# Kernel optimization log

Hardware: AMD Instinct MI355X
Metric: run time of the kernel (lower is better)

Reference implementation:

```python
import jax, jax.numpy as jnp
import numpy as np

B, Q, K, D, H, HD, OUT = 4, 1024, 1024, 256, 8, 32, 256


def setup_inputs() -> dict:
    key = jax.random.key(0)
    ks = jax.random.split(key, 11)
    s = 0.05  # small init scale for weights
    return {
        "q_data": jax.random.normal(ks[0], (B, Q, D), jnp.float32),
        "m_data": jax.random.normal(ks[1], (B, K, D), jnp.float32),
        "bias": jax.random.normal(ks[2], (B, 1, 1, K), jnp.float32),
        "nonbatched_bias": jax.random.normal(ks[3], (H, Q, K), jnp.float32),
        "query_w": jax.random.normal(ks[4], (D, H, HD), jnp.float32) * s,
        "key_w": jax.random.normal(ks[5], (D, H, HD), jnp.float32) * s,
        "value_w": jax.random.normal(ks[6], (D, H, HD), jnp.float32) * s,
        "gating_w": jax.random.normal(ks[7], (D, H, HD), jnp.float32) * s,
        "gating_b": jnp.ones((H, HD), jnp.float32),
        "output_w": jax.random.normal(ks[8], (H, HD, OUT), jnp.float32) * s,
        "output_b": jnp.zeros((OUT,), jnp.float32),
    }


def reference(q_data, m_data, bias, nonbatched_bias, query_w, key_w, value_w,
              gating_w, gating_b, output_w, output_b):
    key_dim = query_w.shape[-1]
    # QKV projections; queries pre-scaled by 1/sqrt(head_dim)
    q = jnp.einsum('bqa,ahc->bqhc', q_data, query_w) * key_dim ** (-0.5)
    k = jnp.einsum('bka,ahc->bkhc', m_data, key_w)
    v = jnp.einsum('bka,ahc->bkhc', m_data, value_w)
    # attention logits [b,h,q,k] plus batched and nonbatched additive biases
    logits_update = jnp.einsum('bqhc,bkhc->bhqk', q, k)
    logits = logits_update + bias + nonbatched_bias[None]
    weights = jax.nn.softmax(logits, axis=-1)
    weighted_avg = jnp.einsum('bhqk,bkhc->bqhc', weights, v)
    # sigmoid gating on the value-aggregated output
    gate = jax.nn.sigmoid(jnp.einsum('bqc,chv->bqhv', q_data, gating_w) + gating_b)
    weighted_avg = weighted_avg * gate
    output = jnp.einsum('bqhc,hco->bqo', weighted_avg, output_w) + output_b
    return (output, logits_update)
```

## Files before the change

kernel.cpp:

```cpp
#include <hip/hip_runtime.h>
#include <hip/hip_bf16.h>

#define NB 4
#define NQ 1024
#define NKS 1024
#define ND 256
#define NH 8
#define NHD 32
#define NOUT 256
#define SPLIT 4

typedef __attribute__((ext_vector_type(8))) short v8s;
typedef __attribute__((ext_vector_type(4))) short v4s;
typedef __attribute__((ext_vector_type(4))) float f32x4;

__global__ __launch_bounds__(256) void prep_all(
    const float* __restrict__ qd, const float* __restrict__ md,
    const float* __restrict__ qw, const float* __restrict__ kw,
    const float* __restrict__ vw, const float* __restrict__ gw,
    const float* __restrict__ ow,
    __hip_bfloat16* __restrict__ Abf, __hip_bfloat16* __restrict__ Wt)
{
  if (blockIdx.x < 1024) {
    const int gid = blockIdx.x * 256 + threadIdx.x;
    const float* src = (gid < 131072) ? qd : md;
    const size_t off = (size_t)(gid & 131071) * 8;
    const float4 a = ((const float4*)(src + off))[0];
    const float4 c = ((const float4*)(src + off))[1];
    __hip_bfloat16 t8[8];
    t8[0]=__float2bfloat16(a.x); t8[1]=__float2bfloat16(a.y);
    t8[2]=__float2bfloat16(a.z); t8[3]=__float2bfloat16(a.w);
    t8[4]=__float2bfloat16(c.x); t8[5]=__float2bfloat16(c.y);
    t8[6]=__float2bfloat16(c.z); t8[7]=__float2bfloat16(c.w);
    *(v8s*)(Abf + (size_t)gid * 8) = *(v8s*)t8;
    return;
  }
  __shared__ float tile[64][65];
  const int wb = blockIdx.x - 1024;
  const int m = wb >> 4, bx = wb & 15;
  const float* src = (m == 0) ? qw : (m == 1) ? kw : (m == 2) ? vw
                   : (m == 3) ? gw : ow;
  const float scale = (m == 0) ? 0.1767766952966369f : 1.0f;
  const int d0 = (bx >> 2) * 64, o0 = (bx & 3) * 64;
  #pragma unroll
  for (int i = 0; i < 16; ++i) {
    const int idx = threadIdx.x + i * 256;
    tile[idx >> 6][idx & 63] = src[(size_t)(d0 + (idx >> 6)) * 256 + o0 + (idx & 63)];
  }
  __syncthreads();
  __hip_bfloat16* dst = Wt + (size_t)m * 65536;
  #pragma unroll
  for (int i = 0; i < 16; ++i) {
    const int idx = threadIdx.x + i * 256;
    const int orow = idx >> 6, dc = idx & 63;
    dst[(size_t)(o0 + orow) * 256 + d0 + dc] = __float2bfloat16(tile[dc][orow] * scale);
  }
}

__global__ __launch_bounds__(256) void proj_kernel(
    const __hip_bfloat16* __restrict__ Abf, const __hip_bfloat16* __restrict__ Wt,
    const float* __restrict__ gating_b,
    __hip_bfloat16* __restrict__ Qw, __hip_bfloat16* __restrict__ Kw,
    __hip_bfloat16* __restrict__ Vt, float* __restrict__ G)
{
  const int wv = threadIdx.x >> 6, lane = threadIdx.x & 63;
  const int c = lane & 15, g = lane >> 4;
  const int task = blockIdx.x * 4 + wv;
  const int ctg = task & 3;
  const int mat = (task >> 2) & 1;
  const int r0g = (task >> 3) & 255;
  const int src = task >> 11;
  const int r0 = r0g * 16;
  const int b = r0 >> 10, pos0 = r0 & 1023;
  const f32x4 z = {0.f, 0.f, 0.f, 0.f};

  const __hip_bfloat16* A = Abf + ((size_t)src * 4096 + r0) * 256;
  v8s af[8];
  #pragma unroll
  for (int ks = 0; ks < 8; ++ks)
    af[ks] = *(const v8s*)(A + c * 256 + ks * 32 + g * 8);

  const int widx = (src == 0) ? (mat ? 3 : 0) : (mat ? 2 : 1);
  const __hip_bfloat16* W = Wt + (size_t)widx * 65536;
  const bool swapped = (src == 1) && (mat == 1);

  f32x4 ac[4] = {z, z, z, z};
  #pragma unroll
  for (int ks = 0; ks < 8; ++ks) {
    #pragma unroll
    for (int j = 0; j < 4; ++j) {
      v8s wf = *(const v8s*)(W + (size_t)((ctg * 4 + j) * 16 + c) * 256 + ks * 32 + g * 8);
      ac[j] = swapped
        ? __builtin_amdgcn_mfma_f32_16x16x32_bf16(wf, af[ks], ac[j], 0, 0, 0)
        : __builtin_amdgcn_mfma_f32_16x16x32_bf16(af[ks], wf, ac[j], 0, 0, 0);
    }
  }

  if (src == 0 && mat == 0) {
    #pragma unroll
    for (int j = 0; j < 4; ++j) {
      const int o = (ctg * 4 + j) * 16 + c, h = o >> 5, hd = o & 31;
      #pragma unroll
      for (int r = 0; r < 4; ++r)
        Qw[((size_t)(b * NH + h) * 1024 + pos0 + 4 * g + r) * 32 + hd] =
            __float2bfloat16(ac[j][r]);
    }
  } else if (src == 0) {
    #pragma unroll
    for (int j = 0; j < 4; ++j) {
      const int o = (ctg * 4 + j) * 16 + c;
      const float gb = gating_b[o];
      #pragma unroll
      for (int r = 0; r < 4; ++r)
        G[(size_t)(r0 + 4 * g + r) * 256 + o] = ac[j][r] + gb;
    }
  } else if (mat == 0) {
    #pragma unroll
    for (int j = 0; j < 4; ++j) {
      const int o = (ctg * 4 + j) * 16 + c, h = o >> 5, hd = o & 31;
      #pragma unroll
      for (int r = 0; r < 4; ++r)
        Kw[((size_t)(b * NH + h) * 1024 + pos0 + 4 * g + r) * 32 + hd] =
            __float2bfloat16(ac[j][r]);
    }
  } else {
    #pragma unroll
    for (int j = 0; j < 4; ++j) {
      #pragma unroll
      for (int r = 0; r < 4; ++r) {
        const int o2 = (ctg * 4 + j) * 16 + 4 * g + r;
        Vt[((size_t)(b * NH + (o2 >> 5)) * 32 + (o2 & 31)) * 1024 + pos0 + c] =
            __float2bfloat16(ac[j][r]);
      }
    }
  }
}

__global__ __launch_bounds__(256) void attn_kernel(
    const __hip_bfloat16* __restrict__ Qw, const __hip_bfloat16* __restrict__ Kw,
    const __hip_bfloat16* __restrict__ Vt,
    const float* __restrict__ bias, const float* __restrict__ nbb,
    float* __restrict__ out_logits,
    __hip_bfloat16* __restrict__ partO, float* __restrict__ partL)
{
  __shared__ __align__(16) __hip_bfloat16 sP[4][16][72];

  const int wv = threadIdx.x >> 6, lane = threadIdx.x & 63;
  const int c = lane & 15, g = lane >> 4;
  const int xcd   = blockIdx.x & 7;
  const int slot  = blockIdx.x >> 3;
  const int bh    = ((slot >> 6) << 3) | xcd;
  const int inner = slot & 63;
  const int sp    = inner >> 4;
  const int qtg   = inner & 15;
  const int qt  = qtg * 4 + wv;
  const int b = bh >> 3, h = bh & 7;
  const int rem = bh * 64 + qt;
  const int q0 = qt * 16;
  const int kbase = sp * (NKS / SPLIT);
  const size_t bhs = (size_t)bh;

  const __hip_bfloat16* Kbase = Kw + bhs * NKS * NHD;
  const __hip_bfloat16* Vbase = Vt + bhs * NHD * NKS;
  const float* biasb = bias + (size_t)b * NKS;
  const float* nbbb  = nbb + ((size_t)h * NQ + q0) * NKS;

  const v8s qfrag = *(const v8s*)(Qw + (bhs * NQ + q0 + c) * NHD + g * 8);

  const f32x4 zacc = {0.f, 0.f, 0.f, 0.f};
  f32x4 O0 = zacc, O1 = zacc;
  float lsumL[4] = {0.f, 0.f, 0.f, 0.f};

  auto loadKV = [&](int k0, v8s* kf, v8s* vf) {
    kf[0] = *(const v8s*)(Kbase + (k0 +      c) * NHD + g * 8);
    kf[1] = *(const v8s*)(Kbase + (k0 + 16 + c) * NHD + g * 8);
    kf[2] = *(const v8s*)(Kbase + (k0 + 32 + c) * NHD + g * 8);
    kf[3] = *(const v8s*)(Kbase + (k0 + 48 + c) * NHD + g * 8);
    vf[0] = *(const v8s*)(Vbase + (     c) * NKS + k0 +      g * 8);
    vf[1] = *(const v8s*)(Vbase + (16 + c) * NKS + k0 +      g * 8);
    vf[2] = *(const v8s*)(Vbase + (     c) * NKS + k0 + 32 + g * 8);
    vf[3] = *(const v8s*)(Vbase + (16 + c) * NKS + k0 + 32 + g * 8);
  };
  auto loadBias = [&](int k0, float* bn) {
    #pragma unroll
    for (int t = 0; t < 4; ++t) {
      const float bvt = biasb[k0 + t * 16 + c];
      #pragma unroll
      for (int r = 0; r < 4; ++r)
        bn[t * 4 + r] = bvt + nbbb[(g * 4 + r) * NKS + k0 + t * 16 + c];
    }
  };

  auto compute = [&](int k0, const v8s* kf, const v8s* vf, const float* bn) {
    f32x4 S[4];
    #pragma unroll
    for (int t = 0; t < 4; ++t)
      S[t] = __builtin_amdgcn_mfma_f32_16x16x32_bf16(qfrag, kf[t], zacc, 0, 0, 0);

    #pragma unroll
    for (int r = 0; r < 4; ++r) {
      const int qrow = q0 + g * 4 + r;
      float* lp = out_logits + (bhs * NQ + qrow) * (size_t)NKS + k0 + c;
      float psum = 0.f;
      #pragma unroll
      for (int t = 0; t < 4; ++t) {
        __builtin_nontemporal_store(S[t][r], lp + t * 16);
        const float p = __expf(S[t][r] + bn[t * 4 + r]);
        psum += p;
        sP[wv][g * 4 + r][t * 16 + c] = __float2bfloat16(p);
      }
      lsumL[r] += psum;
    }

    const v8s pa0 = *(const v8s*)&sP[wv][c][g * 8];
    const v8s pa1 = *(const v8s*)&sP[wv][c][32 + g * 8];
    O0 = __builtin_amdgcn_mfma_f32_16x16x32_bf16(pa0, vf[0], O0, 0, 0, 0);
    O0 = __builtin_amdgcn_mfma_f32_16x16x32_bf16(pa1, vf[2], O0, 0, 0, 0);
    O1 = __builtin_amdgcn_mfma_f32_16x16x32_bf16(pa0, vf[1], O1, 0, 0, 0);
    O1 = __builtin_amdgcn_mfma_f32_16x16x32_bf16(pa1, vf[3], O1, 0, 0, 0);
  };

  v8s kfA[4], vfA[4], kfB[4], vfB[4];
  float bnA[16], bnB[16];

  loadKV(kbase, kfA, vfA);
  loadBias(kbase, bnA);
  #pragma unroll 1
  for (int kt = 0; kt < NKS / SPLIT / 64; kt += 2) {
    loadKV(kbase + (kt + 1) * 64, kfB, vfB);
    loadBias(kbase + (kt + 1) * 64, bnB);
    compute(kbase + kt * 64, kfA, vfA, bnA);
    if (kt + 2 < NKS / SPLIT / 64) {
      loadKV(kbase + (kt + 2) * 64, kfA, vfA);
      loadBias(kbase + (kt + 2) * 64, bnA);
    }
    compute(kbase + (kt + 1) * 64, kfB, vfB, bnB);
  }

  #pragma unroll
  for (int r = 0; r < 4; ++r) {
    float rs = lsumL[r];
    rs += __shfl_xor(rs, 1);
    rs += __shfl_xor(rs, 2);
    rs += __shfl_xor(rs, 4);
    rs += __shfl_xor(rs, 8);
    const int row = 4 * g + r;
    const size_t pb = ((size_t)(rem * SPLIT + sp) * 16 + row) * 32;
    partO[pb + c]      = __float2bfloat16(O0[r]);
    partO[pb + 16 + c] = __float2bfloat16(O1[r]);
    if (c == 0) partL[(size_t)(rem * SPLIT + sp) * 16 + row] = rs;
  }
}

__global__ __launch_bounds__(256) void outproj_kernel(
    const __hip_bfloat16* __restrict__ partO, const float* __restrict__ partL,
    const float* __restrict__ G, const __hip_bfloat16* __restrict__ WtO,
    const float* __restrict__ output_b, float* __restrict__ out)
{
  __shared__ __align__(16) __hip_bfloat16 sRows[16][264];
  const int t = threadIdx.x;
  const int wv = t >> 6, lane = t & 63;
  const int c = lane & 15, g = lane >> 4;
  const int r0 = blockIdx.x * 16;
  const int b = r0 >> 10, qt = (r0 & 1023) >> 4;
  const int h = t >> 5, hd = t & 31;
  const int rem = (b * NH + h) * 64 + qt;

  #pragma unroll 4
  for (int row = 0; row < 16; ++row) {
    float o = 0.f, l = 0.f;
    #pragma unroll
    for (int sp = 0; sp < SPLIT; ++sp) {
      const size_t base = (size_t)(rem * SPLIT + sp) * 16 + row;
      o += __bfloat162float(partO[base * 32 + hd]);
      l += partL[base];
    }
    const float gl = G[(size_t)(r0 + row) * 256 + t];
    sRows[row][t] = __float2bfloat16((o / l) * (1.f / (1.f + __expf(-gl))));
  }
  __syncthreads();

  const f32x4 z = {0.f, 0.f, 0.f, 0.f};
  f32x4 ac[4] = {z, z, z, z};
  #pragma unroll
  for (int ks = 0; ks < 8; ++ks) {
    const v8s af = *(const v8s*)&sRows[c][ks * 32 + g * 8];
    #pragma unroll
    for (int j = 0; j < 4; ++j) {
      const v8s wf = *(const v8s*)(WtO + (size_t)((wv * 4 + j) * 16 + c) * 256 + ks * 32 + g * 8);
      ac[j] = __builtin_amdgcn_mfma_f32_16x16x32_bf16(af, wf, ac[j], 0, 0, 0);
    }
  }
  #pragma unroll
  for (int j = 0; j < 4; ++j) {
    const int o = (wv * 4 + j) * 16 + c;
    const float ob = output_b[o];
    #pragma unroll
    for (int r = 0; r < 4; ++r)
      out[(size_t)(r0 + 4 * g + r) * 256 + o] = ac[j][r] + ob;
  }
}

extern "C" void kernel_launch(void* const* d_in, const int* in_sizes, int n_in,
                              void* d_out, int out_size, void* d_ws, size_t ws_size,
                              hipStream_t stream) {
  const float* q_data   = (const float*)d_in[0];
  const float* m_data   = (const float*)d_in[1];
  const float* bias     = (const float*)d_in[2];
  const float* nbb      = (const float*)d_in[3];
  const float* query_w  = (const float*)d_in[4];
  const float* key_w    = (const float*)d_in[5];
  const float* value_w  = (const float*)d_in[6];
  const float* gating_w = (const float*)d_in[7];
  const float* gating_b = (const float*)d_in[8];
  const float* output_w = (const float*)d_in[9];
  const float* output_b = (const float*)d_in[10];

  float* out        = (float*)d_out;
  float* out_logits = out + (size_t)NB * NQ * NOUT;

  char* ws = (char*)d_ws;
  const size_t MB = 1u << 20;
  __hip_bfloat16* Qw  = (__hip_bfloat16*)(ws);
  __hip_bfloat16* Kw  = (__hip_bfloat16*)(ws + 2 * MB);
  __hip_bfloat16* Vt  = (__hip_bfloat16*)(ws + 4 * MB);
  float*          G   = (float*)(ws + 6 * MB);
  __hip_bfloat16* Abf = (__hip_bfloat16*)(ws + 10 * MB);
  __hip_bfloat16* partO = (__hip_bfloat16*)(ws + 10 * MB);
  float*          partL = (float*)(ws + 19 * MB);
  __hip_bfloat16* Wt  = (__hip_bfloat16*)(ws + 20 * MB);

  prep_all<<<1104, 256, 0, stream>>>(q_data, m_data, query_w, key_w, value_w,
                                     gating_w, output_w, Abf, Wt);
  proj_kernel<<<1024, 256, 0, stream>>>(Abf, Wt, gating_b, Qw, Kw, Vt, G);
  attn_kernel<<<2048, 256, 0, stream>>>(Qw, Kw, Vt, bias, nbb, out_logits, partO, partL);
  outproj_kernel<<<256, 256, 0, stream>>>(partO, partL, G, Wt + (size_t)4 * 65536,
                                          output_b, out);
}
```

Before: 85.33 us.

## Transpose QK^T MFMA so each lane owns one query row for vectorized I/O

The QK^T MFMA operands are swapped so the accumulator comes out transposed: each lane holds four consecutive keys for a single query row instead of four query rows for one key. This turns the logits stores, bias and nonbatched-bias loads, and the P writes to shared memory into 16-byte or 8-byte vector accesses rather than scalar strided ones. The row-sum reduction shrinks to two cross-lane shuffles. The trade-off is a different LDS write pattern for sP, which may cause bank conflicts, and per-lane row addressing that must still match the PV MFMA layout.

```diff
diff --git a/kernel.cpp b/kernel.cpp
--- a/kernel.cpp
+++ b/kernel.cpp
@@ -163,13 +163,14 @@
   const __hip_bfloat16* Kbase = Kw + bhs * NKS * NHD;
   const __hip_bfloat16* Vbase = Vt + bhs * NHD * NKS;
   const float* biasb = bias + (size_t)b * NKS;
-  const float* nbbb  = nbb + ((size_t)h * NQ + q0) * NKS;
+  const float* nbbq  = nbb + ((size_t)h * NQ + q0 + c) * NKS;
+  float*       logq  = out_logits + (bhs * NQ + q0 + c) * (size_t)NKS;
 
   const v8s qfrag = *(const v8s*)(Qw + (bhs * NQ + q0 + c) * NHD + g * 8);
 
   const f32x4 zacc = {0.f, 0.f, 0.f, 0.f};
   f32x4 O0 = zacc, O1 = zacc;
-  float lsumL[4] = {0.f, 0.f, 0.f, 0.f};
+  float lsum = 0.f;
 
   auto loadKV = [&](int k0, v8s* kf, v8s* vf) {
     kf[0] = *(const v8s*)(Kbase + (k0 +      c) * NHD + g * 8);
@@ -181,35 +182,37 @@
     vf[2] = *(const v8s*)(Vbase + (     c) * NKS + k0 + 32 + g * 8);
     vf[3] = *(const v8s*)(Vbase + (16 + c) * NKS + k0 + 32 + g * 8);
   };
-  auto loadBias = [&](int k0, float* bn) {
+  auto loadBias = [&](int k0, f32x4* bn) {
     #pragma unroll
     for (int t = 0; t < 4; ++t) {
-      const float bvt = biasb[k0 + t * 16 + c];
-      #pragma unroll
-      for (int r = 0; r < 4; ++r)
-        bn[t * 4 + r] = bvt + nbbb[(g * 4 + r) * NKS + k0 + t * 16 + c];
+      const f32x4 b4 = *(const f32x4*)(biasb + k0 + t * 16 + 4 * g);
+      const f32x4 n4 = *(const f32x4*)(nbbq  + k0 + t * 16 + 4 * g);
+      bn[t] = b4 + n4;
     }
   };
 
-  auto compute = [&](int k0, const v8s* kf, const v8s* vf, const float* bn) {
+  auto compute = [&](int k0, const v8s* kf, const v8s* vf, const f32x4* bn) {
     f32x4 S[4];
     #pragma unroll
     for (int t = 0; t < 4; ++t)
-      S[t] = __builtin_amdgcn_mfma_f32_16x16x32_bf16(qfrag, kf[t], zacc, 0, 0, 0);
-
-    #pragma unroll
-    for (int r = 0; r < 4; ++r) {
-      const int qrow = q0 + g * 4 + r;
-      float* lp = out_logits + (bhs * NQ + qrow) * (size_t)NKS + k0 + c;
-      float psum = 0.f;
-      #pragma unroll
-      for (int t = 0; t < 4; ++t) {
-        __builtin_nontemporal_store(S[t][r], lp + t * 16);
-        const float p = __expf(S[t][r] + bn[t * 4 + r]);
-        psum += p;
-        sP[wv][g * 4 + r][t * 16 + c] = __float2bfloat16(p);
+      S[t] = __builtin_amdgcn_mfma_f32_16x16x32_bf16(kf[t], qfrag, zacc, 0, 0, 0);
+
+    #pragma unroll
+    for (int t = 0; t < 4; ++t) {
+      __builtin_nontemporal_store(S[t], (f32x4*)(logq + k0 + t * 16 + 4 * g));
+      const f32x4 e = S[t] + bn[t];
+      float p[4];
+      short4 s4;
+      #pragma unroll
+      for (int r = 0; r < 4; ++r) {
+        p[r] = __expf(e[r]);
+        lsum += p[r];
       }
-      lsumL[r] += psum;
+      s4.x = (short)__bfloat16_as_ushort(__float2bfloat16(p[0]));
+      s4.y = (short)__bfloat16_as_ushort(__float2bfloat16(p[1]));
+      s4.z = (short)__bfloat16_as_ushort(__float2bfloat16(p[2]));
+      s4.w = (short)__bfloat16_as_ushort(__float2bfloat16(p[3]));
+      *(short4*)&sP[wv][c][t * 16 + 4 * g] = s4;
     }
 
     const v8s pa0 = *(const v8s*)&sP[wv][c][g * 8];
@@ -221,7 +224,7 @@
   };
 
   v8s kfA[4], vfA[4], kfB[4], vfB[4];
-  float bnA[16], bnB[16];
+  f32x4 bnA[4], bnB[4];
 
   loadKV(kbase, kfA, vfA);
   loadBias(kbase, bnA);
@@ -237,18 +240,18 @@
     compute(kbase + (kt + 1) * 64, kfB, vfB, bnB);
   }
 
+  float rs = lsum;
+  rs += __shfl_xor(rs, 16);
+  rs += __shfl_xor(rs, 32);
+  if (lane < 16)
+    partL[(size_t)(rem * SPLIT + sp) * 16 + lane] = rs;
+
   #pragma unroll
   for (int r = 0; r < 4; ++r) {
-    float rs = lsumL[r];
-    rs += __shfl_xor(rs, 1);
-    rs += __shfl_xor(rs, 2);
-    rs += __shfl_xor(rs, 4);
-    rs += __shfl_xor(rs, 8);
     const int row = 4 * g + r;
     const size_t pb = ((size_t)(rem * SPLIT + sp) * 16 + row) * 32;
     partO[pb + c]      = __float2bfloat16(O0[r]);
     partO[pb + 16 + c] = __float2bfloat16(O1[r]);
-    if (c == 0) partL[(size_t)(rem * SPLIT + sp) * 16 + row] = rs;
   }
 }
 
```

Result: slower. 91.13 us (+6.8%).
